# Kernel optimization log

Hardware: AMD Instinct MI355X
Metric: run time of the kernel (lower is better)

## Reference

```python
import jax, jax.numpy as jnp
import numpy as np
from itertools import product

D = 128        # input voxel grid side
N_IN = 150000  # active input voxels
C_IN = 32
C_OUT = 64
M = 100000     # active output voxels kept after stride-2 downsample
EPS = 1e-5


def _build_rulebooks():
    rng = np.random.default_rng(0)
    flat = rng.choice(D ** 3, size=N_IN, replace=False)
    coords = np.stack(np.unravel_index(flat, (D, D, D)), axis=1).astype(np.int64)  # [N_IN,3]
    # SparseConv3d(kernel=2, stride=2, padding=1): input i contributes to output o with
    # i = 2*o - 1 + k, k in {0,1}; per dim exactly one k is valid -> o = (i+1)//2.
    out_all = (coords + 1) // 2
    koff = (coords + 1) % 2
    kidx = koff[:, 0] * 4 + koff[:, 1] * 2 + koff[:, 2]
    out_coords, inv = np.unique(out_all, axis=0, return_inverse=True)
    assert len(out_coords) >= M, 'not enough occupied parent voxels'
    out_coords = out_coords[:M]
    nbr_down = -np.ones((M, 8), np.int32)
    sel = inv < M
    nbr_down[inv[sel], kidx[sel]] = np.arange(N_IN, dtype=np.int32)[sel]
    # SubMConv3d(kernel=3, padding=1): output sites == input sites; neighbor table per offset.
    S = 67  # hash stride (out coords in [0,65), +1 shift keeps neighbor keys in range)
    key = (out_coords[:, 0] + 1) * S * S + (out_coords[:, 1] + 1) * S + (out_coords[:, 2] + 1)
    lut = -np.ones(S ** 3, np.int32)
    lut[key] = np.arange(M, dtype=np.int32)
    nbr_sub = np.empty((M, 27), np.int32)
    for k, (dx, dy, dz) in enumerate(product((-1, 0, 1), repeat=3)):
        nbr_sub[:, k] = lut[key + dx * S * S + dy * S + dz]
    return nbr_down, nbr_sub


def setup_inputs() -> dict:
    nbr_down, nbr_sub = _build_rulebooks()
    key = jax.random.key(0)
    k0, k1, k2, k3, k4 = jax.random.split(key, 5)
    ones = jnp.ones((C_OUT,), jnp.float32)
    zeros = jnp.zeros((C_OUT,), jnp.float32)
    return {
        'x_feats': jax.random.normal(k0, (N_IN, C_IN), jnp.float32),
        'w_down': jax.random.normal(k1, (8, C_IN, C_OUT), jnp.float32) / np.sqrt(8 * C_IN),
        'g_down': ones, 'b_down': zeros,
        'w_proj': jax.random.normal(k2, (C_OUT, C_OUT), jnp.float32) / np.sqrt(C_OUT),
        'g_p': ones, 'b_p': zeros,
        'w1': jax.random.normal(k3, (27, C_OUT, C_OUT), jnp.float32) / np.sqrt(27 * C_OUT),
        'g1': ones, 'b1': zeros,
        'w2': jax.random.normal(k4, (27, C_OUT, C_OUT), jnp.float32) / np.sqrt(27 * C_OUT),
        'g2': ones, 'b2': zeros,
        'nbr_down': jnp.asarray(nbr_down),
        'nbr_sub': jnp.asarray(nbr_sub),
    }


def _bn(f, g, b):
    # BatchNorm1d in training mode over the active-voxel dim (biased variance)
    m = f.mean(0)
    v = jnp.mean((f - m) ** 2, 0)
    return (f - m) * jax.lax.rsqrt(v + EPS) * g + b


def _spconv(feats, nbr, W):
    # rulebook gather-GEMM-scatter: out[m] = sum_k feats[nbr[m,k]] @ W[k]  (nbr=-1 -> zero)
    n = feats.shape[0]
    fpad = jnp.concatenate([feats, jnp.zeros((1, feats.shape[1]), feats.dtype)], axis=0)
    idx = jnp.where(nbr < 0, n, nbr)
    out = jnp.zeros((nbr.shape[0], W.shape[2]), feats.dtype)
    for k in range(W.shape[0]):  # fixed small kernel volume (8 or 27)
        out = out + fpad[idx[:, k]] @ W[k]
    return out


def reference(x_feats, w_down, g_down, b_down, w_proj, g_p, b_p,
              w1, g1, b1, w2, g2, b2, nbr_down, nbr_sub):
    # DonwBlock.down: SparseConv3d -> BN -> ReLU
    x = jax.nn.relu(_bn(_spconv(x_feats, nbr_down, w_down), g_down, b_down))
    # DoubleConv.proj: 1x1 SubMConv (plain linear on features) -> BN
    res = _bn(x @ w_proj, g_p, b_p)
    # conv1 -> bn1 -> relu -> conv2 -> bn2 -> +proj -> relu
    out = jax.nn.relu(_bn(_spconv(x, nbr_sub, w1), g1, b1))
    out = _bn(_spconv(out, nbr_sub, w2), g2, b2) + res
    return jax.nn.relu(out)
```

## Files before the change

kernel.cpp:

```cpp
#include <hip/hip_runtime.h>

static constexpr int M_ROWS = 100000;
static constexpr int N_IN   = 150000;
static constexpr int C_IN   = 32;
static constexpr int CO     = 64;
static constexpr float EPS  = 1e-5f;

typedef __bf16 bf16x8 __attribute__((ext_vector_type(8)));
typedef float  f32x4  __attribute__((ext_vector_type(4)));
typedef unsigned short u16x8 __attribute__((ext_vector_type(8)));
typedef short  short8 __attribute__((ext_vector_type(8)));
typedef unsigned int u32;

static __device__ __forceinline__ unsigned short f2bf(float f) {
    unsigned int u = __builtin_bit_cast(unsigned int, f);
    u += 0x7fff + ((u >> 16) & 1);
    return (unsigned short)(u >> 16);
}
static __device__ __forceinline__ float bf2f(unsigned short h) {
    unsigned int u = ((unsigned int)h) << 16;
    return __builtin_bit_cast(float, u);
}

static __device__ __forceinline__ void gload_lds16(const void* g, void* l) {
    __builtin_amdgcn_global_load_lds(
        (const __attribute__((address_space(1))) u32*)g,
        (__attribute__((address_space(3))) u32*)l, 16, 0, 0);
}

__global__ __launch_bounds__(256) void cvt_bf16(
    const float* __restrict__ in, unsigned short* __restrict__ out, int n8)
{
    int i = blockIdx.x * 256 + threadIdx.x;
    if (i >= n8) return;
    float4 a = ((const float4*)in)[2 * i];
    float4 b = ((const float4*)in)[2 * i + 1];
    u16x8 v;
    v[0] = f2bf(a.x); v[1] = f2bf(a.y); v[2] = f2bf(a.z); v[3] = f2bf(a.w);
    v[4] = f2bf(b.x); v[5] = f2bf(b.y); v[6] = f2bf(b.z); v[7] = f2bf(b.w);
    ((u16x8*)out)[i] = v;
}

__global__ __launch_bounds__(256) void wt_cvt_swz(
    const float* __restrict__ W, unsigned short* __restrict__ WT, int total, int cin)
{
    int t = blockIdx.x * 256 + threadIdx.x;
    if (t >= total) return;
    int k  = t / (cin * 64);
    int r  = t - k * (cin * 64);
    int ci = r >> 6;
    int co = r & 63;
    int xm = (cin == 64) ? ((co & 7) << 4) : ((co & 3) << 4);
    int phys = co * (cin * 2) + ((ci * 2) ^ xm);
    WT[(size_t)k * cin * 64 + (phys >> 1)] = f2bf(W[t]);
}

template<int CIN, int KOFF, int ST, bool GATHER, bool OUTBF>
__global__ __launch_bounds__(256, 2) void spconv_mfma(
    const unsigned short* __restrict__ fB,
    int nZero,
    const int*   __restrict__ nbr,
    const unsigned short* __restrict__ WTs,
    void* __restrict__ outp,
    float* __restrict__ part)
{
    constexpr int KS    = CIN / 32;
    constexpr int SLAB  = CIN * 64;
    constexpr int REPS  = (SLAB * 2) / 4096;
    constexpr int ROWSB = 4 * ST * 16;

    __shared__ unsigned short Wl[2][SLAB];
    __shared__ int nbrS[GATHER ? ROWSB * KOFF : 4];
    __shared__ float red[4][2][64];

    const int tid  = threadIdx.x;
    const int lane = tid & 63;
    const int wv   = tid >> 6;
    const int colb = lane & 15;
    const int kgrp = lane >> 4;

    const int nwg = gridDim.x;
    const int q   = nwg >> 3, r8 = nwg & 7;
    const int xcd = blockIdx.x & 7, pos = blockIdx.x >> 3;
    const int wg  = (xcd < r8 ? xcd * (q + 1) : r8 * (q + 1) + (xcd - r8) * q) + pos;
    const int m0  = wg * ROWSB;

    auto stageW = [&](int k, int b) {
        const unsigned short* g = WTs + (size_t)k * SLAB;
        #pragma unroll
        for (int r = 0; r < REPS; ++r) {
            const void* gp = g + (size_t)(r * 256 + tid) * 8;
            void* lp = &Wl[b][(size_t)(r * 256 + wv * 64) * 8];
            gload_lds16(gp, lp);
        }
    };

    stageW(0, 0);
    if (GATHER) {
        const int* src = nbr + (size_t)m0 * KOFF;
        constexpr int TOT = ROWSB * KOFF;
        if (m0 + ROWSB <= M_ROWS) {
            #pragma unroll 1
            for (int i = tid; i < TOT / 4; i += 256)
                ((int4*)nbrS)[i] = ((const int4*)src)[i];
        } else {
            #pragma unroll 1
            for (int i = tid; i < TOT; i += 256) {
                int r = i / KOFF;
                nbrS[i] = (m0 + r < M_ROWS) ? src[i] : -1;
            }
        }
    }
    __syncthreads();

    auto gatherA = [&](int k, bf16x8 (&dst)[ST][KS]) {
        #pragma unroll
        for (int st = 0; st < ST; ++st) {
            int rloc = wv * (ST * 16) + st * 16 + colb;
            int idx;
            if (GATHER) idx = nbrS[rloc * KOFF + k];
            else        idx = (m0 + rloc < M_ROWS) ? (m0 + rloc) : -1;
            if (idx < 0) idx = nZero;
            const unsigned short* fp = fB + (size_t)idx * CIN + kgrp * 8;
            #pragma unroll
            for (int s = 0; s < KS; ++s)
                dst[st][s] = *reinterpret_cast<const bf16x8*>(fp + s * 32);
        }
    };

    f32x4 acc[ST][4] = {};

    auto compute = [&](int buf, const bf16x8 (&a)[ST][KS]) {
        bf16x8 w[4][KS];
        const char* base = (const char*)&Wl[0][0] + (size_t)buf * SLAB * 2;
        #pragma unroll
        for (int n = 0; n < 4; ++n) {
            int r  = n * 16 + colb;
            int xm = (CIN == 64) ? ((r & 7) << 4) : ((r & 3) << 4);
            #pragma unroll
            for (int s = 0; s < KS; ++s) {
                int c2 = kgrp * 16 + s * 64;
                int phys = r * (CIN * 2) + (c2 ^ xm);
                w[n][s] = *reinterpret_cast<const bf16x8*>(base + phys);
            }
        }
        #pragma unroll
        for (int st = 0; st < ST; ++st)
            #pragma unroll
            for (int n = 0; n < 4; ++n)
                #pragma unroll
                for (int s = 0; s < KS; ++s)
                    acc[st][n] = __builtin_amdgcn_mfma_f32_16x16x32_bf16(
                        a[st][s], w[n][s], acc[st][n], 0, 0, 0);
    };

    #pragma unroll 1
    for (int k = 0; k < KOFF; ++k) {
        bf16x8 a[ST][KS];
        gatherA(k, a);
        if (k + 1 < KOFF) stageW(k + 1, (k + 1) & 1);
        compute(k & 1, a);
        if (k + 1 < KOFF) __syncthreads();
    }

    #pragma unroll
    for (int st = 0; st < ST; ++st) {
        int rbase = m0 + wv * (ST * 16) + st * 16 + kgrp * 4;
        #pragma unroll
        for (int j = 0; j < 4; ++j) {
            int row = rbase + j;
            if (row < M_ROWS) {
                if (OUTBF) {
                    unsigned short* o = (unsigned short*)outp;
                    #pragma unroll
                    for (int n = 0; n < 4; ++n)
                        o[(size_t)row * 64 + n * 16 + colb] = f2bf(acc[st][n][j]);
                } else {
                    float* o = (float*)outp;
                    #pragma unroll
                    for (int n = 0; n < 4; ++n)
                        o[(size_t)row * 64 + n * 16 + colb] = acc[st][n][j];
                }
            }
        }
    }

    float s4[4], q4[4];
    #pragma unroll
    for (int n = 0; n < 4; ++n) {
        float s = 0.f, qq = 0.f;
        #pragma unroll
        for (int st = 0; st < ST; ++st)
            #pragma unroll
            for (int j = 0; j < 4; ++j) {
                float v = acc[st][n][j];
                s += v; qq += v * v;
            }
        s4[n] = s; q4[n] = qq;
    }
    #pragma unroll
    for (int n = 0; n < 4; ++n) {
        s4[n] += __shfl_xor(s4[n], 16); s4[n] += __shfl_xor(s4[n], 32);
        q4[n] += __shfl_xor(q4[n], 16); q4[n] += __shfl_xor(q4[n], 32);
    }
    if (kgrp == 0) {
        #pragma unroll
        for (int n = 0; n < 4; ++n) {
            red[wv][0][n * 16 + colb] = s4[n];
            red[wv][1][n * 16 + colb] = q4[n];
        }
    }
    __syncthreads();
    if (tid < 64) {
        float S = red[0][0][tid] + red[1][0][tid] + red[2][0][tid] + red[3][0][tid];
        float Q = red[0][1][tid] + red[1][1][tid] + red[2][1][tid] + red[3][1][tid];
        part[(size_t)wg * 128 + tid]      = S;
        part[(size_t)wg * 128 + 64 + tid] = Q;
    }
}

__global__ __launch_bounds__(1024) void bn_finalize(
    const float* __restrict__ part, int nblocks,
    const float* __restrict__ gg, const float* __restrict__ bb,
    float* __restrict__ ss, int M)
{
    const int tid = threadIdx.x;
    const int c   = tid & 63;
    const int grp = tid >> 6;
    float S = 0.f, Q = 0.f;
    int i = grp;
    for (; i + 48 < nblocks; i += 64) {
        float a0 = part[(size_t)(i     ) * 128 + c];
        float a1 = part[(size_t)(i + 16) * 128 + c];
        float a2 = part[(size_t)(i + 32) * 128 + c];
        float a3 = part[(size_t)(i + 48) * 128 + c];
        float q0 = part[(size_t)(i     ) * 128 + 64 + c];
        float q1 = part[(size_t)(i + 16) * 128 + 64 + c];
        float q2 = part[(size_t)(i + 32) * 128 + 64 + c];
        float q3 = part[(size_t)(i + 48) * 128 + 64 + c];
        S += a0 + a1 + a2 + a3;
        Q += q0 + q1 + q2 + q3;
    }
    for (; i < nblocks; i += 16) {
        S += part[(size_t)i * 128 + c];
        Q += part[(size_t)i * 128 + 64 + c];
    }
    __shared__ float sh[2][16][64];
    sh[0][grp][c] = S; sh[1][grp][c] = Q;
    __syncthreads();
    if (tid < 64) {
        float Sa = 0.f, Qa = 0.f;
        #pragma unroll
        for (int j = 0; j < 16; ++j) { Sa += sh[0][j][tid]; Qa += sh[1][j][tid]; }
        float mean = Sa / (float)M;
        float var  = Qa / (float)M - mean * mean;
        float rstd = rsqrtf(var + EPS);
        float sc = gg[tid] * rstd;
        ss[tid]      = sc;
        ss[64 + tid] = bb[tid] - mean * sc;
    }
}

template<bool INBF, bool BF16OUT, bool RES, bool RELU>
__global__ __launch_bounds__(256) void bn_apply(
    const void* __restrict__ yp, const float* __restrict__ ss,
    const unsigned short* __restrict__ res, void* __restrict__ out, int n8)
{
    for (int i = blockIdx.x * 256 + threadIdx.x; i < n8; i += gridDim.x * 256) {
        float v[8];
        if (INBF) {
            u16x8 u = ((const u16x8*)yp)[i];
            #pragma unroll
            for (int j = 0; j < 8; ++j) v[j] = bf2f(u[j]);
        } else {
            float4 a = ((const float4*)yp)[2 * i];
            float4 b = ((const float4*)yp)[2 * i + 1];
            v[0] = a.x; v[1] = a.y; v[2] = a.z; v[3] = a.w;
            v[4] = b.x; v[5] = b.y; v[6] = b.z; v[7] = b.w;
        }
        int c0 = (i * 8) & 63;
        #pragma unroll
        for (int j = 0; j < 8; ++j)
            v[j] = v[j] * ss[c0 + j] + ss[64 + c0 + j];
        if (RES) {
            u16x8 rv = ((const u16x8*)res)[i];
            #pragma unroll
            for (int j = 0; j < 8; ++j) v[j] += bf2f(rv[j]);
        }
        if (RELU) {
            #pragma unroll
            for (int j = 0; j < 8; ++j) v[j] = fmaxf(v[j], 0.f);
        }
        if (BF16OUT) {
            u16x8 o;
            #pragma unroll
            for (int j = 0; j < 8; ++j) o[j] = f2bf(v[j]);
            ((u16x8*)out)[i] = o;
        } else {
            float4 oa, ob;
            oa.x = v[0]; oa.y = v[1]; oa.z = v[2]; oa.w = v[3];
            ob.x = v[4]; ob.y = v[5]; ob.z = v[6]; ob.w = v[7];
            ((float4*)out)[2 * i]     = oa;
            ((float4*)out)[2 * i + 1] = ob;
        }
    }
}

extern "C" void kernel_launch(void* const* d_in, const int* in_sizes, int n_in,
                              void* d_out, int out_size, void* d_ws, size_t ws_size,
                              hipStream_t stream)
{
    const float* x_feats = (const float*)d_in[0];
    const float* w_down  = (const float*)d_in[1];
    const float* g_down  = (const float*)d_in[2];
    const float* b_down  = (const float*)d_in[3];
    const float* w_proj  = (const float*)d_in[4];
    const float* g_p     = (const float*)d_in[5];
    const float* b_p     = (const float*)d_in[6];
    const float* w1      = (const float*)d_in[7];
    const float* g1      = (const float*)d_in[8];
    const float* b1      = (const float*)d_in[9];
    const float* w2      = (const float*)d_in[10];
    const float* g2      = (const float*)d_in[11];
    const float* b2      = (const float*)d_in[12];
    const int*   nbr_down = (const int*)d_in[13];
    const int*   nbr_sub  = (const int*)d_in[14];
    float* out = (float*)d_out;

    const int M = M_ROWS;
    const int conv_grid = (M + 255) / 256;
    const size_t feat4 = (size_t)M * CO * 4;
    const size_t feat2 = (size_t)(M + 1) * CO * 2;
    auto align = [](size_t x) { return (x + 255) & ~(size_t)255; };

    char* ws = (char*)d_ws;
    size_t off = 0;
    unsigned short* xin16 = (unsigned short*)(ws + off); off += align((size_t)(N_IN + 1) * C_IN * 2);
    unsigned short* wdT   = (unsigned short*)(ws + off); off += align((size_t)8 * CO * C_IN * 2);
    unsigned short* wpT   = (unsigned short*)(ws + off); off += align((size_t)1 * CO * CO * 2);
    unsigned short* w1T   = (unsigned short*)(ws + off); off += align((size_t)27 * CO * CO * 2);
    unsigned short* w2T   = (unsigned short*)(ws + off); off += align((size_t)27 * CO * CO * 2);
    float* Y    = (float*)(ws + off); off += align(feat4);
    unsigned short* bufRb = (unsigned short*)(ws + off); off += align(feat2);
    unsigned short* xB = (unsigned short*)(ws + off); off += align(feat2);
    unsigned short* zB = (unsigned short*)(ws + off); off += align(feat2);
    float* part = (float*)(ws + off); off += align((size_t)1024 * 128 * 4);
    float* ss0  = (float*)(ws + off);
    float* ss1  = ss0 + 128;
    float* ss2  = ss1 + 128;
    float* ss3  = ss2 + 128;

    unsigned short* Yb = (unsigned short*)Y;

    const int n8 = M * CO / 8;
    const int ew_grid = 2048;

    hipMemsetAsync(xin16 + (size_t)N_IN * C_IN, 0, C_IN * 2, stream);
    hipMemsetAsync(xB + (size_t)M * CO, 0, CO * 2, stream);
    hipMemsetAsync(zB + (size_t)M * CO, 0, CO * 2, stream);

    {
        int nf8 = N_IN * C_IN / 8;
        cvt_bf16<<<(nf8 + 255) / 256, 256, 0, stream>>>(x_feats, xin16, nf8);
        int t;
        t = 8 * C_IN * CO;  wt_cvt_swz<<<(t + 255) / 256, 256, 0, stream>>>(w_down, wdT, t, C_IN);
        t = CO * CO;        wt_cvt_swz<<<(t + 255) / 256, 256, 0, stream>>>(w_proj, wpT, t, CO);
        t = 27 * CO * CO;   wt_cvt_swz<<<(t + 255) / 256, 256, 0, stream>>>(w1, w1T, t, CO);
        t = 27 * CO * CO;   wt_cvt_swz<<<(t + 255) / 256, 256, 0, stream>>>(w2, w2T, t, CO);
    }

    spconv_mfma<C_IN, 8, 4, true, true><<<conv_grid, 256, 0, stream>>>(
        xin16, N_IN, nbr_down, wdT, Yb, part);
    bn_finalize<<<1, 1024, 0, stream>>>(part, conv_grid, g_down, b_down, ss0, M);
    bn_apply<true, true, false, true><<<ew_grid, 256, 0, stream>>>(Yb, ss0, nullptr, xB, n8);

    spconv_mfma<CO, 1, 4, false, true><<<conv_grid, 256, 0, stream>>>(
        xB, M, nullptr, wpT, Yb, part);
    bn_finalize<<<1, 1024, 0, stream>>>(part, conv_grid, g_p, b_p, ss1, M);
    bn_apply<true, true, false, false><<<ew_grid, 256, 0, stream>>>(Yb, ss1, nullptr, bufRb, n8);

    spconv_mfma<CO, 27, 4, true, true><<<conv_grid, 256, 0, stream>>>(
        xB, M, nbr_sub, w1T, Yb, part);
    bn_finalize<<<1, 1024, 0, stream>>>(part, conv_grid, g1, b1, ss2, M);
    bn_apply<true, true, false, true><<<ew_grid, 256, 0, stream>>>(Yb, ss2, nullptr, zB, n8);

    spconv_mfma<CO, 27, 4, true, false><<<conv_grid, 256, 0, stream>>>(
        zB, M, nbr_sub, w2T, Y, part);
    bn_finalize<<<1, 1024, 0, stream>>>(part, conv_grid, g2, b2, ss3, M);
    bn_apply<false, false, true, true><<<ew_grid, 256, 0, stream>>>(Y, ss3, bufRb, out, n8);
}
```

Measured before the change: 182.3 us.

## Stage weight slabs in phases of eight and halve rows per block

```diff
diff --git a/kernel.cpp b/kernel.cpp
--- a/kernel.cpp
+++ b/kernel.cpp
@@ -55,7 +55,7 @@
     WT[(size_t)k * cin * 64 + (phys >> 1)] = f2bf(W[t]);
 }
 
-template<int CIN, int KOFF, int ST, bool GATHER, bool OUTBF>
+template<int CIN, int KOFF, int PH, bool GATHER, bool OUTBF>
 __global__ __launch_bounds__(256, 2) void spconv_mfma(
     const unsigned short* __restrict__ fB,
     int nZero,
@@ -65,12 +65,14 @@
     float* __restrict__ part)
 {
     constexpr int KS    = CIN / 32;
+    constexpr int ST    = 2;
     constexpr int SLAB  = CIN * 64;
-    constexpr int REPS  = (SLAB * 2) / 4096;
-    constexpr int ROWSB = 4 * ST * 16;
-
-    __shared__ unsigned short Wl[2][SLAB];
-    __shared__ int nbrS[GATHER ? ROWSB * KOFF : 4];
+    constexpr int P1    = (KOFF < PH) ? KOFF : PH;
+    constexpr int NF    = KOFF / PH;
+    constexpr int T     = KOFF - NF * PH;
+
+    __shared__ unsigned short Wl[P1 * SLAB];
+    __shared__ int nbrS[GATHER ? 128 * KOFF : 4];
     __shared__ float red[4][2][64];
 
     const int tid  = threadIdx.x;
@@ -83,23 +85,23 @@
     const int q   = nwg >> 3, r8 = nwg & 7;
     const int xcd = blockIdx.x & 7, pos = blockIdx.x >> 3;
     const int wg  = (xcd < r8 ? xcd * (q + 1) : r8 * (q + 1) + (xcd - r8) * q) + pos;
-    const int m0  = wg * ROWSB;
-
-    auto stageW = [&](int k, int b) {
-        const unsigned short* g = WTs + (size_t)k * SLAB;
-        #pragma unroll
-        for (int r = 0; r < REPS; ++r) {
+    const int m0  = wg * 128;
+
+    auto stageN = [&](int k0, int cnt) {
+        const unsigned short* g = WTs + (size_t)k0 * SLAB;
+        const int reps = cnt * (SLAB / 2048);
+        for (int r = 0; r < reps; ++r) {
             const void* gp = g + (size_t)(r * 256 + tid) * 8;
-            void* lp = &Wl[b][(size_t)(r * 256 + wv * 64) * 8];
+            void* lp = &Wl[(size_t)(r * 256 + wv * 64) * 8];
             gload_lds16(gp, lp);
         }
     };
 
-    stageW(0, 0);
+    stageN(0, P1);
     if (GATHER) {
         const int* src = nbr + (size_t)m0 * KOFF;
-        constexpr int TOT = ROWSB * KOFF;
-        if (m0 + ROWSB <= M_ROWS) {
+        constexpr int TOT = 128 * KOFF;
+        if (m0 + 128 <= M_ROWS) {
             #pragma unroll 1
             for (int i = tid; i < TOT / 4; i += 256)
                 ((int4*)nbrS)[i] = ((const int4*)src)[i];
@@ -130,9 +132,9 @@
 
     f32x4 acc[ST][4] = {};
 
-    auto compute = [&](int buf, const bf16x8 (&a)[ST][KS]) {
+    auto compute = [&](int slab, const bf16x8 (&a)[ST][KS]) {
         bf16x8 w[4][KS];
-        const char* base = (const char*)&Wl[0][0] + (size_t)buf * SLAB * 2;
+        const char* base = (const char*)&Wl[0] + (size_t)slab * SLAB * 2;
         #pragma unroll
         for (int n = 0; n < 4; ++n) {
             int r  = n * 16 + colb;
@@ -155,12 +157,27 @@
     };
 
     #pragma unroll 1
-    for (int k = 0; k < KOFF; ++k) {
-        bf16x8 a[ST][KS];
-        gatherA(k, a);
-        if (k + 1 < KOFF) stageW(k + 1, (k + 1) & 1);
-        compute(k & 1, a);
-        if (k + 1 < KOFF) __syncthreads();
+    for (int p = 0; p < NF; ++p) {
+        const int k0 = p * PH;
+        #pragma unroll
+        for (int kk = 0; kk < PH; ++kk) {
+            bf16x8 a[ST][KS];
+            gatherA(k0 + kk, a);
+            compute(kk, a);
+        }
+        if (p + 1 < NF || T > 0) {
+            __syncthreads();
+            stageN((p + 1) * PH, (p + 1 < NF) ? PH : T);
+            __syncthreads();
+        }
+    }
+    if (T > 0) {
+        #pragma unroll
+        for (int kk = 0; kk < T; ++kk) {
+            bf16x8 a[ST][KS];
+            gatherA(NF * PH + kk, a);
+            compute(kk, a);
+        }
     }
 
     #pragma unroll
@@ -328,7 +345,7 @@
     float* out = (float*)d_out;
 
     const int M = M_ROWS;
-    const int conv_grid = (M + 255) / 256;
+    const int conv_grid = (M + 127) / 128;
     const size_t feat4 = (size_t)M * CO * 4;
     const size_t feat2 = (size_t)(M + 1) * CO * 2;
     auto align = [](size_t x) { return (x + 255) & ~(size_t)255; };
@@ -369,22 +386,22 @@
         t = 27 * CO * CO;   wt_cvt_swz<<<(t + 255) / 256, 256, 0, stream>>>(w2, w2T, t, CO);
     }
 
-    spconv_mfma<C_IN, 8, 4, true, true><<<conv_grid, 256, 0, stream>>>(
+    spconv_mfma<C_IN, 8, 8, true, true><<<conv_grid, 256, 0, stream>>>(
         xin16, N_IN, nbr_down, wdT, Yb, part);
     bn_finalize<<<1, 1024, 0, stream>>>(part, conv_grid, g_down, b_down, ss0, M);
     bn_apply<true, true, false, true><<<ew_grid, 256, 0, stream>>>(Yb, ss0, nullptr, xB, n8);
 
-    spconv_mfma<CO, 1, 4, false, true><<<conv_grid, 256, 0, stream>>>(
+    spconv_mfma<CO, 1, 1, false, true><<<conv_grid, 256, 0, stream>>>(
         xB, M, nullptr, wpT, Yb, part);
     bn_finalize<<<1, 1024, 0, stream>>>(part, conv_grid, g_p, b_p, ss1, M);
     bn_apply<true, true, false, false><<<ew_grid, 256, 0, stream>>>(Yb, ss1, nullptr, bufRb, n8);
 
-    spconv_mfma<CO, 27, 4, true, true><<<conv_grid, 256, 0, stream>>>(
+    spconv_mfma<CO, 27, 8, true, true><<<conv_grid, 256, 0, stream>>>(
         xB, M, nbr_sub, w1T, Yb, part);
     bn_finalize<<<1, 1024, 0, stream>>>(part, conv_grid, g1, b1, ss2, M);
     bn_apply<true, true, false, true><<<ew_grid, 256, 0, stream>>>(Yb, ss2, nullptr, zB, n8);
 
-    spconv_mfma<CO, 27, 4, true, false><<<conv_grid, 256, 0, stream>>>(
+    spconv_mfma<CO, 27, 8, true, false><<<conv_grid, 256, 0, stream>>>(
         zB, M, nbr_sub, w2T, Y, part);
     bn_finalize<<<1, 1024, 0, stream>>>(part, conv_grid, g2, b2, ss3, M);
     bn_apply<false, false, true, true><<<ew_grid, 256, 0, stream>>>(Y, ss3, bufRb, out, n8);
```

Result: slower. 196.6 us (+7.8%).
